# Kernel optimization log

Hardware: AMD Instinct MI355X
Metric: run time of the kernel (lower is better)

The kernel has to match this reference:

```python
import jax, jax.numpy as jnp
import numpy as np

BLOCK = 64
CRIT_TH = 0.5
NEGL_TH = 0.01
TEMP = 1.0
EPS = 1e-6


def setup_inputs() -> dict:
    key = jax.random.key(0)
    kq, kk, kv = jax.random.split(key, 3)
    B, T, H, D = 1, 2048, 8, 64
    q = jax.random.normal(kq, (B, T, H, D), dtype=jnp.float32)
    k = jax.random.normal(kk, (B, T, H, D), dtype=jnp.float32)
    v = jax.random.normal(kv, (B, T, H, D), dtype=jnp.float32)
    return {"q": q, "k": k, "v": v}


def _classify_blocks(qb, kb, D):
    # qb: [B,nq,bs,H,D], kb: [B,nk,bs,H,D]
    q_rep = qb.mean(axis=2)  # [B,nq,H,D]
    k_rep = kb.mean(axis=2)  # [B,nk,H,D]
    bscores = jnp.einsum('bqhd,bkhd->bhqk', q_rep, k_rep) / np.float32(np.sqrt(D))
    ssm = jax.nn.softmax(bscores, axis=-1)
    var = jnp.var(ssm, axis=-1, ddof=1, keepdims=True)  # unbiased, matches torch .var()
    max_scores = bscores.max(axis=-1, keepdims=True)
    imp = var * jnp.maximum(max_scores - bscores.min(), EPS)
    imp_n = (imp - imp.min()) / (imp.max() - imp.min() + EPS)
    crit = imp_n >= CRIT_TH
    negl = imp_n <= NEGL_TH
    marg = (~crit) & (~negl)
    return crit, marg


def reference(q, k, v):
    B, T, H, D = q.shape
    S = k.shape[1]
    nq, nk = T // BLOCK, S // BLOCK  # T,S are multiples of BLOCK (no padding needed)
    dtype = q.dtype

    qb = q.reshape(B, nq, BLOCK, H, D)
    kb = k.reshape(B, nk, BLOCK, H, D)
    vb = v.reshape(B, nk, BLOCK, H, D)

    crit, marg = _classify_blocks(qb, kb, D)  # [B,H,nq,nk] bool
    critf = crit.astype(dtype)
    margf = marg.astype(dtype)

    # ---- exact (critical) blocks: per-block-pair softmax attention ----
    scale = np.float32(1.0 / (np.sqrt(D) * TEMP))
    scores = jnp.einsum('bqthd,bkshd->bhqkts', qb, kb) * scale  # [B,H,nq,nk,bs,bs]
    attn = jax.nn.softmax(scores.astype(jnp.float32), axis=-1).astype(dtype)
    attn_m = attn * critf[:, :, :, :, None, None]
    out_c = jnp.einsum('bhqkts,bkshd->bqthd', attn_m, vb)  # [B,nq,bs,H,D]
    w_c = jnp.einsum('bhqkts->bqth', attn_m)[..., None]    # [B,nq,bs,H,1]

    # ---- linear (marginal) blocks: ELU+1 feature-map attention ----
    qf = jax.nn.elu(qb / TEMP) + 1.0
    kf = jax.nn.elu(kb / TEMP) + 1.0
    kv = jnp.einsum('bkshd,bkshv->bkhdv', kf, vb)              # [B,nk,H,D,D]
    num = jnp.einsum('bqthd,bkhdv->bqkthv', qf, kv)            # [B,nq,nk,bs,H,D]
    k_sum = kf.sum(axis=2)                                     # [B,nk,H,D]
    den = jnp.einsum('bqthd,bkhd->bqkth', qf, k_sum) + EPS     # [B,nq,nk,bs,H]
    out_pair = num / den[..., None]
    out_l = jnp.einsum('bqkthd,bhqk->bqthd', out_pair, margf)
    w_l = jnp.einsum('bqkth,bhqk->bqth', den, margf)[..., None]

    out = (out_c + out_l) / (w_c + w_l + EPS)
    return out.reshape(B, T, H, D)
```

## Files before the change

kernel.cpp:

```cpp
#include <hip/hip_runtime.h>
#include <math.h>

namespace {
constexpr int H  = 8;
constexpr int D  = 64;
constexpr int NB = 32;
constexpr int BS = 64;
constexpr int QST = 68;
}
#define FEPS 1e-6f

typedef unsigned short u16;
typedef unsigned int   u32;
typedef __attribute__((ext_vector_type(8))) short bf16x8;
typedef __attribute__((ext_vector_type(4))) float floatx4;

__device__ __forceinline__ u32 f2bf(float x) {
  union { float f; u32 u; } v; v.f = x;
  return (v.u + 0x7FFFu + ((v.u >> 16) & 1u)) >> 16;
}
__device__ __forceinline__ u32 pk2(float a, float b) { return f2bf(a) | (f2bf(b) << 16); }
#define ELU1(x) ((x) > 0.f ? (x) + 1.f : expf(x))
#define SWZ(row, kblk) ((row)*64 + (((kblk) ^ ((row)&7))*8))

__global__ __launch_bounds__(256) void prep_kernel(const float* __restrict__ q,
                                                   const float* __restrict__ k,
                                                   const float* __restrict__ v,
                                                   float* __restrict__ kvt,
                                                   float* __restrict__ ksum,
                                                   double* __restrict__ qrep,
                                                   double* __restrict__ krep) {
  __shared__ float smem[3*BS*D];
  int bid = blockIdx.x;
  int tid = threadIdx.x;
  if (bid >= 256) {
    double* qred = (double*)smem;
    int r = bid - 256;
    int h = r >> 5, bi = r & 31;
    int d = tid & 63, quarter = tid >> 6;
    double s = 0.0;
    for (int t = quarter*16; t < quarter*16 + 16; ++t)
      s += (double)q[((bi*BS + t)*H + h)*D + d];
    qred[quarter*64 + d] = s;
    __syncthreads();
    if (tid < 64)
      qrep[r*D + tid] = (qred[tid] + qred[64+tid] + qred[128+tid] + qred[192+tid]) * (1.0/64.0);
    return;
  }
  float* kf   = smem;
  float* vv   = smem + BS*D;
  float* kraw = smem + 2*BS*D;
  int h = bid >> 5, ki = bid & 31;
  int sr = tid >> 2, cg = tid & 3;
  const float4* kb = (const float4*)(k + ((ki*BS + sr)*H + h)*D);
  const float4* vb = (const float4*)(v + ((ki*BS + sr)*H + h)*D);
#pragma unroll
  for (int m = 0; m < 4; ++m) {
    float4 kk = kb[cg*4 + m];
    float4 vx = vb[cg*4 + m];
    int c = cg*16 + m*4;
    *(float4*)&kraw[sr*D + c] = kk;
    kf[sr*D + c + 0] = ELU1(kk.x);
    kf[sr*D + c + 1] = ELU1(kk.y);
    kf[sr*D + c + 2] = ELU1(kk.z);
    kf[sr*D + c + 3] = ELU1(kk.w);
    *(float4*)&vv[sr*D + c] = vx;
  }
  __syncthreads();
  int c = tid & 63, dg = tid >> 6, d0 = dg*16;
  float acc[16];
#pragma unroll
  for (int j = 0; j < 16; ++j) acc[j] = 0.f;
#pragma unroll 4
  for (int s2 = 0; s2 < BS; ++s2) {
    float vval = vv[s2*D + c];
    const float4* kr = (const float4*)&kf[s2*D + d0];
    float4 a0 = kr[0], a1 = kr[1], a2 = kr[2], a3 = kr[3];
    acc[0]  += vval*a0.x; acc[1]  += vval*a0.y; acc[2]  += vval*a0.z; acc[3]  += vval*a0.w;
    acc[4]  += vval*a1.x; acc[5]  += vval*a1.y; acc[6]  += vval*a1.z; acc[7]  += vval*a1.w;
    acc[8]  += vval*a2.x; acc[9]  += vval*a2.y; acc[10] += vval*a2.z; acc[11] += vval*a2.w;
    acc[12] += vval*a3.x; acc[13] += vval*a3.y; acc[14] += vval*a3.z; acc[15] += vval*a3.w;
  }
  float* op = kvt + (size_t)bid*4096 + c*64 + d0;
  *(float4*)(op + 0)  = make_float4(acc[0],  acc[1],  acc[2],  acc[3]);
  *(float4*)(op + 4)  = make_float4(acc[4],  acc[5],  acc[6],  acc[7]);
  *(float4*)(op + 8)  = make_float4(acc[8],  acc[9],  acc[10], acc[11]);
  *(float4*)(op + 12) = make_float4(acc[12], acc[13], acc[14], acc[15]);
  if (dg == 0) {
    float ks = 0.f;
    for (int s2 = 0; s2 < BS; ++s2) ks += kf[s2*D + c];
    ksum[bid*D + c] = ks;
    double m = 0.0;
    for (int s2 = 0; s2 < BS; ++s2) m += (double)kraw[s2*D + c];
    krep[bid*D + c] = m * (1.0/64.0);
  }
}

__global__ __launch_bounds__(256) void bscore_kernel(const double* __restrict__ qrep,
                                                     const double* __restrict__ krep,
                                                     double* __restrict__ bsc) {
  int tid = threadIdx.x;
  int lr = tid >> 5, ki = tid & 31;
  int r = blockIdx.x * 8 + lr;
  int h = r >> 5;
  const double* qr = qrep + r*D;
  const double* kr = krep + (h*NB + ki)*D;
  double s = 0.0;
#pragma unroll 16
  for (int d = 0; d < D; ++d) s += qr[d]*kr[d];
  bsc[r*NB + ki] = s * 0.125;
}

__global__ __launch_bounds__(256) void classify3_kernel(const double* __restrict__ bsc,
                                                        int* __restrict__ flags) {
  __shared__ double red[256];
  int tid = threadIdx.x;
  const double* row = bsc + tid*NB;
  double rmax = -1.0e300, rmin = 1.0e300;
#pragma unroll 8
  for (int i = 0; i < NB; ++i) { double b = row[i]; rmax = fmax(rmax, b); rmin = fmin(rmin, b); }
  red[tid] = rmin; __syncthreads();
  for (int s = 128; s > 0; s >>= 1) { if (tid < s) red[tid] = fmin(red[tid], red[tid+s]); __syncthreads(); }
  double gmin = red[0]; __syncthreads();
  double S = 0.0, S2 = 0.0;
#pragma unroll 8
  for (int i = 0; i < NB; ++i) { double e = exp(row[i] - rmax); S += e; S2 += e*e; }
  double invS = 1.0 / S;
  double sp = S * invS;
  double mu = sp * (1.0/32.0);
  double var = (S2*invS*invS - 2.0*mu*sp + 32.0*mu*mu) * (1.0/31.0);
  double rng = rmax - gmin;
  if (rng < 1e-6) rng = 1e-6;
  double imp = var * rng;
  red[tid] = imp; __syncthreads();
  for (int s = 128; s > 0; s >>= 1) { if (tid < s) red[tid] = fmin(red[tid], red[tid+s]); __syncthreads(); }
  double imin = red[0]; __syncthreads();
  red[tid] = imp; __syncthreads();
  for (int s = 128; s > 0; s >>= 1) { if (tid < s) red[tid] = fmax(red[tid], red[tid+s]); __syncthreads(); }
  double imax = red[0];
  double impn = (imp - imin) / (imax - imin + 1e-6);
  flags[tid] = (impn >= 0.5) ? 2 : ((impn <= 0.01) ? 0 : 1);
}

__global__ __launch_bounds__(256) void main_kernel(
    const float* __restrict__ q, const float* __restrict__ k, const float* __restrict__ v,
    const float* __restrict__ kvt, const float* __restrict__ ksum,
    const int* __restrict__ flags, float* __restrict__ out) {
  __shared__ float smem[10304];
  int bid = blockIdx.x;
  int h = bid >> 5, qi = bid & 31;
  int tid = threadIdx.x;
  int row = tid >> 2, cg = tid & 3, c0 = cg*16;
  int lane = tid & 63;
  int flag = flags[bid];

  if (flag == 1) {
    u16*  qfb  = (u16*)smem;
    u16*  kvb  = (u16*)(smem + 2048);
    float* idens = smem + 6144;
    float* wsl   = smem + 8192;
    float* kslc  = smem + 8256;

    {
      const float4* kss = (const float4*)(ksum + (size_t)(h*NB)*D);
      for (int i = tid; i < NB*16; i += 256) ((float4*)kslc)[i] = kss[i];
    }
    float qf[16];
    {
      const float4* qp = (const float4*)(q + ((qi*BS + row)*H + h)*D + c0);
      float4 q0 = qp[0], q1 = qp[1], q2 = qp[2], q3 = qp[3];
      qf[0]=ELU1(q0.x); qf[1]=ELU1(q0.y); qf[2]=ELU1(q0.z); qf[3]=ELU1(q0.w);
      qf[4]=ELU1(q1.x); qf[5]=ELU1(q1.y); qf[6]=ELU1(q1.z); qf[7]=ELU1(q1.w);
      qf[8]=ELU1(q2.x); qf[9]=ELU1(q2.y); qf[10]=ELU1(q2.z); qf[11]=ELU1(q2.w);
      qf[12]=ELU1(q3.x); qf[13]=ELU1(q3.y); qf[14]=ELU1(q3.z); qf[15]=ELU1(q3.w);
      uint4 p0, p1;
      p0.x = pk2(qf[0],qf[1]);  p0.y = pk2(qf[2],qf[3]);
      p0.z = pk2(qf[4],qf[5]);  p0.w = pk2(qf[6],qf[7]);
      p1.x = pk2(qf[8],qf[9]);  p1.y = pk2(qf[10],qf[11]);
      p1.z = pk2(qf[12],qf[13]); p1.w = pk2(qf[14],qf[15]);
      *(uint4*)&qfb[SWZ(row, cg*2)]     = p0;
      *(uint4*)&qfb[SWZ(row, cg*2 + 1)] = p1;
    }
    const float* kvbase = kvt + (size_t)(h*NB)*4096 + row*64 + c0;
    float4 t0, t1, t2, t3;
    {
      const float4* kvp = (const float4*)kvbase;
      t0 = kvp[0]; t1 = kvp[1]; t2 = kvp[2]; t3 = kvp[3];
    }
    __syncthreads();
    {
      float wloc = 0.f;
      for (int ki = 0; ki < NB; ++ki) {
        float pd = 0.f;
#pragma unroll
        for (int j = 0; j < 16; ++j) pd += qf[j] * kslc[ki*64 + c0 + j];
        pd += __shfl_xor(pd, 1, 64);
        pd += __shfl_xor(pd, 2, 64);
        float den = pd + FEPS;
        if (cg == 0) idens[row*32 + ki] = 1.0f / den;
        wloc += den;
      }
      if (cg == 0) wsl[row] = wloc;
    }
    {
      uint4 p0, p1;
      p0.x = pk2(t0.x,t0.y); p0.y = pk2(t0.z,t0.w);
      p0.z = pk2(t1.x,t1.y); p0.w = pk2(t1.z,t1.w);
      p1.x = pk2(t2.x,t2.y); p1.y = pk2(t2.z,t2.w);
      p1.z = pk2(t3.x,t3.y); p1.w = pk2(t3.z,t3.w);
      *(uint4*)&kvb[SWZ(row, cg*2)]     = p0;
      *(uint4*)&kvb[SWZ(row, cg*2 + 1)] = p1;
    }
    int w = tid >> 6, m = lane & 15, quad = lane >> 4;
    bf16x8 aLo = *(const bf16x8*)&qfb[SWZ(w*16 + m, quad)];
    bf16x8 aHi = *(const bf16x8*)&qfb[SWZ(w*16 + m, 4 + quad)];
    int rbase = w*16 + quad*4;
    float acc[16];
#pragma unroll
    for (int j = 0; j < 16; ++j) acc[j] = 0.f;

    for (int ki = 0; ki < NB; ++ki) {
      if (ki + 1 < NB) {
        const float4* kvp = (const float4*)(kvbase + (size_t)(ki+1)*4096);
        t0 = kvp[0]; t1 = kvp[1]; t2 = kvp[2]; t3 = kvp[3];
      }
      __syncthreads();
      const u16* kb = kvb + (ki & 1)*4096;
      float i0 = idens[(rbase + 0)*32 + ki];
      float i1 = idens[(rbase + 1)*32 + ki];
      float i2 = idens[(rbase + 2)*32 + ki];
      float i3 = idens[(rbase + 3)*32 + ki];
      floatx4 zz = {0.f, 0.f, 0.f, 0.f};
#pragma unroll
      for (int t = 0; t < 4; ++t) {
        bf16x8 bLo = *(const bf16x8*)&kb[SWZ(t*16 + m, quad)];
        bf16x8 bHi = *(const bf16x8*)&kb[SWZ(t*16 + m, 4 + quad)];
        floatx4 c4 = __builtin_amdgcn_mfma_f32_16x16x32_bf16(aLo, bLo, zz, 0, 0, 0);
        c4 = __builtin_amdgcn_mfma_f32_16x16x32_bf16(aHi, bHi, c4, 0, 0, 0);
        acc[t*4+0] += c4[0]*i0;
        acc[t*4+1] += c4[1]*i1;
        acc[t*4+2] += c4[2]*i2;
        acc[t*4+3] += c4[3]*i3;
      }
      if (ki + 1 < NB) {
        u16* kw = kvb + ((ki+1) & 1)*4096;
        uint4 p0, p1;
        p0.x = pk2(t0.x,t0.y); p0.y = pk2(t0.z,t0.w);
        p0.z = pk2(t1.x,t1.y); p0.w = pk2(t1.z,t1.w);
        p1.x = pk2(t2.x,t2.y); p1.y = pk2(t2.z,t2.w);
        p1.z = pk2(t3.x,t3.y); p1.w = pk2(t3.z,t3.w);
        *(uint4*)&kw[SWZ(row, cg*2)]     = p0;
        *(uint4*)&kw[SWZ(row, cg*2 + 1)] = p1;
      }
    }
#pragma unroll
    for (int r = 0; r < 4; ++r) {
      float wd = 1.0f / (wsl[rbase + r] + FEPS);
      float* op = out + ((qi*BS + rbase + r)*H + h)*D + m;
#pragma unroll
      for (int t = 0; t < 4; ++t) op[t*16] = acc[t*4+r]*wd;
    }
    return;
  }

  float* bufA = smem;
  float* bufB = smem + 4352;
  float acc[16];
#pragma unroll
  for (int j = 0; j < 16; ++j) acc[j] = 0.f;
  float wsum = 0.f;

  if (flag == 2) {
    const float4* qp = (const float4*)(q + ((qi*BS + row)*H + h)*D);
#pragma unroll
    for (int mm = 0; mm < 4; ++mm) {
      float4 qq = qp[cg*4 + mm];
      int c = c0 + mm*4;
      bufA[row*QST + c + 0] = qq.x*0.125f;
      bufA[row*QST + c + 1] = qq.y*0.125f;
      bufA[row*QST + c + 2] = qq.z*0.125f;
      bufA[row*QST + c + 3] = qq.w*0.125f;
    }
    __syncthreads();
    for (int ki = 0; ki < NB; ++ki) {
      const float4* kp = (const float4*)(k + ((ki*BS + row)*H + h)*D);
#pragma unroll
      for (int mm = 0; mm < 4; ++mm)
        *(float4*)&bufB[row*QST + c0 + mm*4] = kp[cg*4 + mm];
      __syncthreads();
      float sc[16];
#pragma unroll
      for (int j = 0; j < 16; ++j) sc[j] = 0.f;
      for (int d = 0; d < D; ++d) {
        float a = bufA[row*QST + d];
#pragma unroll
        for (int j = 0; j < 16; ++j)
          sc[j] += a * bufB[(c0 + j)*QST + d];
      }
      float mx = sc[0];
#pragma unroll
      for (int j = 1; j < 16; ++j) mx = fmaxf(mx, sc[j]);
      mx = fmaxf(mx, __shfl_xor(mx, 1, 64));
      mx = fmaxf(mx, __shfl_xor(mx, 2, 64));
      float es = 0.f;
      float p[16];
#pragma unroll
      for (int j = 0; j < 16; ++j) { p[j] = expf(sc[j] - mx); es += p[j]; }
      es += __shfl_xor(es, 1, 64);
      es += __shfl_xor(es, 2, 64);
      float inv = 1.0f / es;
#pragma unroll
      for (int j = 0; j < 16; ++j) p[j] *= inv;
      wsum += es * inv;
      __syncthreads();
      const float4* vp = (const float4*)(v + ((ki*BS + row)*H + h)*D);
#pragma unroll
      for (int mm = 0; mm < 4; ++mm)
        *(float4*)&bufB[row*QST + c0 + mm*4] = vp[cg*4 + mm];
      __syncthreads();
      for (int s2 = 0; s2 < BS; ++s2) {
        int g = s2 >> 4, jj = s2 & 15;
        float pv = __shfl(p[jj], (lane & ~3) | g, 64);
        const float4* vr = (const float4*)&bufB[s2*QST + c0];
        float4 a0 = vr[0], a1 = vr[1], a2 = vr[2], a3 = vr[3];
        acc[0]  += pv*a0.x; acc[1]  += pv*a0.y; acc[2]  += pv*a0.z; acc[3]  += pv*a0.w;
        acc[4]  += pv*a1.x; acc[5]  += pv*a1.y; acc[6]  += pv*a1.z; acc[7]  += pv*a1.w;
        acc[8]  += pv*a2.x; acc[9]  += pv*a2.y; acc[10] += pv*a2.z; acc[11] += pv*a2.w;
        acc[12] += pv*a3.x; acc[13] += pv*a3.y; acc[14] += pv*a3.z; acc[15] += pv*a3.w;
      }
      __syncthreads();
    }
  }
  float wd = 1.0f / (wsum + FEPS);
  float* op = out + ((qi*BS + row)*H + h)*D + c0;
  *(float4*)(op + 0)  = make_float4(acc[0]*wd,  acc[1]*wd,  acc[2]*wd,  acc[3]*wd);
  *(float4*)(op + 4)  = make_float4(acc[4]*wd,  acc[5]*wd,  acc[6]*wd,  acc[7]*wd);
  *(float4*)(op + 8)  = make_float4(acc[8]*wd,  acc[9]*wd,  acc[10]*wd, acc[11]*wd);
  *(float4*)(op + 12) = make_float4(acc[12]*wd, acc[13]*wd, acc[14]*wd, acc[15]*wd);
}

extern "C" void kernel_launch(void* const* d_in, const int* in_sizes, int n_in,
                              void* d_out, int out_size, void* d_ws, size_t ws_size,
                              hipStream_t stream) {
  const float* q = (const float*)d_in[0];
  const float* k = (const float*)d_in[1];
  const float* v = (const float*)d_in[2];
  float* out = (float*)d_out;
  char* ws = (char*)d_ws;
  double* qrep = (double*)(ws + 0);
  double* krep = (double*)(ws + 131072);
  int*    flg  = (int*)   (ws + 262144);
  float*  ksw  = (float*) (ws + 263168);
  float*  kvw  = (float*) (ws + 328704);
  double* bsc  = (double*)(ws + 4523008);

  prep_kernel<<<512, 256, 0, stream>>>(q, k, v, kvw, ksw, qrep, krep);
  bscore_kernel<<<32, 256, 0, stream>>>(qrep, krep, bsc);
  classify3_kernel<<<1, 256, 0, stream>>>(bsc, flg);
  main_kernel<<<256, 256, 0, stream>>>(q, k, v, kvw, ksw, flg, out);
}
```

Before: 109.7 us.

## Fuse four kernels into one cooperative kernel with grid syncs

Merges the prep, block-score, classify and main kernels into a single cooperative launch of 256 blocks, separated by two grid-wide barriers. Block scores and row statistics are now computed per block in shared memory. Each block then redoes the global min/max reduction over 256 rows itself, instead of one block classifying everything. The aim is to remove three kernel launch gaps and the intermediate global round-trips; the cost is grid-sync overhead and the constraint that all 256 blocks stay co-resident.

```diff
diff --git a/kernel.cpp b/kernel.cpp
--- a/kernel.cpp
+++ b/kernel.cpp
@@ -1,5 +1,8 @@
 #include <hip/hip_runtime.h>
+#include <hip/hip_cooperative_groups.h>
 #include <math.h>
+
+namespace cg = cooperative_groups;
 
 namespace {
 constexpr int H  = 8;
@@ -23,136 +26,159 @@
 #define ELU1(x) ((x) > 0.f ? (x) + 1.f : expf(x))
 #define SWZ(row, kblk) ((row)*64 + (((kblk) ^ ((row)&7))*8))
 
-__global__ __launch_bounds__(256) void prep_kernel(const float* __restrict__ q,
-                                                   const float* __restrict__ k,
-                                                   const float* __restrict__ v,
-                                                   float* __restrict__ kvt,
-                                                   float* __restrict__ ksum,
-                                                   double* __restrict__ qrep,
-                                                   double* __restrict__ krep) {
-  __shared__ float smem[3*BS*D];
+__global__ __launch_bounds__(256) void fused_kernel(
+    const float* __restrict__ q, const float* __restrict__ k, const float* __restrict__ v,
+    float* __restrict__ kvt, float* __restrict__ ksum, double* __restrict__ krep,
+    double* __restrict__ rowmin, double* __restrict__ rowmax, double* __restrict__ rowvar,
+    float* __restrict__ out) {
+  cg::grid_group grid = cg::this_grid();
+  __shared__ __align__(16) float smem[12288];
   int bid = blockIdx.x;
   int tid = threadIdx.x;
-  if (bid >= 256) {
-    double* qred = (double*)smem;
-    int r = bid - 256;
-    int h = r >> 5, bi = r & 31;
+  int h = bid >> 5, qi = bid & 31;
+
+  {
+    float* kf   = smem;
+    float* vv   = smem + 4096;
+    float* kraw = smem + 8192;
+    int sr = tid >> 2, cgp = tid & 3;
+    const float4* kb = (const float4*)(k + ((qi*BS + sr)*H + h)*D);
+    const float4* vb = (const float4*)(v + ((qi*BS + sr)*H + h)*D);
+#pragma unroll
+    for (int m = 0; m < 4; ++m) {
+      float4 kk = kb[cgp*4 + m];
+      float4 vx = vb[cgp*4 + m];
+      int c = cgp*16 + m*4;
+      *(float4*)&kraw[sr*D + c] = kk;
+      kf[sr*D + c + 0] = ELU1(kk.x);
+      kf[sr*D + c + 1] = ELU1(kk.y);
+      kf[sr*D + c + 2] = ELU1(kk.z);
+      kf[sr*D + c + 3] = ELU1(kk.w);
+      *(float4*)&vv[sr*D + c] = vx;
+    }
+    __syncthreads();
+    int c = tid & 63, dg = tid >> 6, d0 = dg*16;
+    float acc[16];
+#pragma unroll
+    for (int j = 0; j < 16; ++j) acc[j] = 0.f;
+#pragma unroll 4
+    for (int s2 = 0; s2 < BS; ++s2) {
+      float vval = vv[s2*D + c];
+      const float4* kr = (const float4*)&kf[s2*D + d0];
+      float4 a0 = kr[0], a1 = kr[1], a2 = kr[2], a3 = kr[3];
+      acc[0]  += vval*a0.x; acc[1]  += vval*a0.y; acc[2]  += vval*a0.z; acc[3]  += vval*a0.w;
+      acc[4]  += vval*a1.x; acc[5]  += vval*a1.y; acc[6]  += vval*a1.z; acc[7]  += vval*a1.w;
+      acc[8]  += vval*a2.x; acc[9]  += vval*a2.y; acc[10] += vval*a2.z; acc[11] += vval*a2.w;
+      acc[12] += vval*a3.x; acc[13] += vval*a3.y; acc[14] += vval*a3.z; acc[15] += vval*a3.w;
+    }
+    float* op = kvt + (size_t)bid*4096 + c*64 + d0;
+    *(float4*)(op + 0)  = make_float4(acc[0],  acc[1],  acc[2],  acc[3]);
+    *(float4*)(op + 4)  = make_float4(acc[4],  acc[5],  acc[6],  acc[7]);
+    *(float4*)(op + 8)  = make_float4(acc[8],  acc[9],  acc[10], acc[11]);
+    *(float4*)(op + 12) = make_float4(acc[12], acc[13], acc[14], acc[15]);
+    if (dg == 0) {
+      float ks = 0.f;
+      for (int s2 = 0; s2 < BS; ++s2) ks += kf[s2*D + c];
+      ksum[bid*D + c] = ks;
+      double m = 0.0;
+      for (int s2 = 0; s2 < BS; ++s2) m += (double)kraw[s2*D + c];
+      krep[bid*D + c] = m * (1.0/64.0);
+    }
+  }
+  __syncthreads();
+
+  double* qred  = (double*)smem;
+  double* qrepL = (double*)(smem + 512);
+  {
     int d = tid & 63, quarter = tid >> 6;
     double s = 0.0;
     for (int t = quarter*16; t < quarter*16 + 16; ++t)
-      s += (double)q[((bi*BS + t)*H + h)*D + d];
+      s += (double)q[((qi*BS + t)*H + h)*D + d];
     qred[quarter*64 + d] = s;
     __syncthreads();
     if (tid < 64)
-      qrep[r*D + tid] = (qred[tid] + qred[64+tid] + qred[128+tid] + qred[192+tid]) * (1.0/64.0);
-    return;
-  }
-  float* kf   = smem;
-  float* vv   = smem + BS*D;
-  float* kraw = smem + 2*BS*D;
-  int h = bid >> 5, ki = bid & 31;
-  int sr = tid >> 2, cg = tid & 3;
-  const float4* kb = (const float4*)(k + ((ki*BS + sr)*H + h)*D);
-  const float4* vb = (const float4*)(v + ((ki*BS + sr)*H + h)*D);
-#pragma unroll
-  for (int m = 0; m < 4; ++m) {
-    float4 kk = kb[cg*4 + m];
-    float4 vx = vb[cg*4 + m];
-    int c = cg*16 + m*4;
-    *(float4*)&kraw[sr*D + c] = kk;
-    kf[sr*D + c + 0] = ELU1(kk.x);
-    kf[sr*D + c + 1] = ELU1(kk.y);
-    kf[sr*D + c + 2] = ELU1(kk.z);
-    kf[sr*D + c + 3] = ELU1(kk.w);
-    *(float4*)&vv[sr*D + c] = vx;
+      qrepL[tid] = (qred[tid] + qred[64+tid] + qred[128+tid] + qred[192+tid]) * (1.0/64.0);
+    __syncthreads();
+  }
+  __threadfence();
+  grid.sync();
+
+  {
+    double* partb = (double*)(smem + 1024);
+    double* bsrow = (double*)(smem + 1536);
+    int ki = tid & 31, seg = tid >> 5;
+    const double* kr = krep + (size_t)(h*NB + ki)*D + seg*8;
+    double s = 0.0;
+#pragma unroll
+    for (int j = 0; j < 8; ++j) s += qrepL[seg*8 + j] * kr[j];
+    partb[tid] = s;
+    __syncthreads();
+    if (tid < 32) {
+      double s2 = 0.0;
+#pragma unroll
+      for (int g = 0; g < 8; ++g) s2 += partb[g*32 + tid];
+      bsrow[tid] = s2 * 0.125;
+    }
+    __syncthreads();
+    if (tid < 64) {
+      double b = bsrow[tid & 31];
+      double rmax = b, rmin = b;
+#pragma unroll
+      for (int m = 1; m < 32; m <<= 1) {
+        rmax = fmax(rmax, __shfl_xor(rmax, m, 64));
+        rmin = fmin(rmin, __shfl_xor(rmin, m, 64));
+      }
+      double e = exp(b - rmax);
+      double S = e, S2 = e*e;
+#pragma unroll
+      for (int m = 1; m < 32; m <<= 1) {
+        S  += __shfl_xor(S,  m, 64);
+        S2 += __shfl_xor(S2, m, 64);
+      }
+      if (tid == 0) {
+        double invS = 1.0 / S;
+        double sp = S * invS;
+        double mu = sp * (1.0/32.0);
+        double var = (S2*invS*invS - 2.0*mu*sp + 32.0*mu*mu) * (1.0/31.0);
+        rowmin[bid] = rmin;
+        rowmax[bid] = rmax;
+        rowvar[bid] = var;
+      }
+    }
+  }
+  __threadfence();
+  grid.sync();
+
+  int flag;
+  {
+    double* buf  = (double*)smem;
+    double* impL = (double*)(smem + 512);
+    buf[tid] = rowmin[tid];
+    __syncthreads();
+    for (int s = 128; s > 0; s >>= 1) { if (tid < s) buf[tid] = fmin(buf[tid], buf[tid+s]); __syncthreads(); }
+    double gmin = buf[0];
+    __syncthreads();
+    double rng = rowmax[tid] - gmin;
+    if (rng < 1e-6) rng = 1e-6;
+    double imp = rowvar[tid] * rng;
+    impL[tid] = imp;
+    buf[tid] = imp;
+    __syncthreads();
+    for (int s = 128; s > 0; s >>= 1) { if (tid < s) buf[tid] = fmin(buf[tid], buf[tid+s]); __syncthreads(); }
+    double imin = buf[0];
+    __syncthreads();
+    buf[tid] = imp;
+    __syncthreads();
+    for (int s = 128; s > 0; s >>= 1) { if (tid < s) buf[tid] = fmax(buf[tid], buf[tid+s]); __syncthreads(); }
+    double imax = buf[0];
+    __syncthreads();
+    double impn = (impL[bid] - imin) / (imax - imin + 1e-6);
+    flag = (impn >= 0.5) ? 2 : ((impn <= 0.01) ? 0 : 1);
   }
   __syncthreads();
-  int c = tid & 63, dg = tid >> 6, d0 = dg*16;
-  float acc[16];
-#pragma unroll
-  for (int j = 0; j < 16; ++j) acc[j] = 0.f;
-#pragma unroll 4
-  for (int s2 = 0; s2 < BS; ++s2) {
-    float vval = vv[s2*D + c];
-    const float4* kr = (const float4*)&kf[s2*D + d0];
-    float4 a0 = kr[0], a1 = kr[1], a2 = kr[2], a3 = kr[3];
-    acc[0]  += vval*a0.x; acc[1]  += vval*a0.y; acc[2]  += vval*a0.z; acc[3]  += vval*a0.w;
-    acc[4]  += vval*a1.x; acc[5]  += vval*a1.y; acc[6]  += vval*a1.z; acc[7]  += vval*a1.w;
-    acc[8]  += vval*a2.x; acc[9]  += vval*a2.y; acc[10] += vval*a2.z; acc[11] += vval*a2.w;
-    acc[12] += vval*a3.x; acc[13] += vval*a3.y; acc[14] += vval*a3.z; acc[15] += vval*a3.w;
-  }
-  float* op = kvt + (size_t)bid*4096 + c*64 + d0;
-  *(float4*)(op + 0)  = make_float4(acc[0],  acc[1],  acc[2],  acc[3]);
-  *(float4*)(op + 4)  = make_float4(acc[4],  acc[5],  acc[6],  acc[7]);
-  *(float4*)(op + 8)  = make_float4(acc[8],  acc[9],  acc[10], acc[11]);
-  *(float4*)(op + 12) = make_float4(acc[12], acc[13], acc[14], acc[15]);
-  if (dg == 0) {
-    float ks = 0.f;
-    for (int s2 = 0; s2 < BS; ++s2) ks += kf[s2*D + c];
-    ksum[bid*D + c] = ks;
-    double m = 0.0;
-    for (int s2 = 0; s2 < BS; ++s2) m += (double)kraw[s2*D + c];
-    krep[bid*D + c] = m * (1.0/64.0);
-  }
-}
-
-__global__ __launch_bounds__(256) void bscore_kernel(const double* __restrict__ qrep,
-                                                     const double* __restrict__ krep,
-                                                     double* __restrict__ bsc) {
-  int tid = threadIdx.x;
-  int lr = tid >> 5, ki = tid & 31;
-  int r = blockIdx.x * 8 + lr;
-  int h = r >> 5;
-  const double* qr = qrep + r*D;
-  const double* kr = krep + (h*NB + ki)*D;
-  double s = 0.0;
-#pragma unroll 16
-  for (int d = 0; d < D; ++d) s += qr[d]*kr[d];
-  bsc[r*NB + ki] = s * 0.125;
-}
-
-__global__ __launch_bounds__(256) void classify3_kernel(const double* __restrict__ bsc,
-                                                        int* __restrict__ flags) {
-  __shared__ double red[256];
-  int tid = threadIdx.x;
-  const double* row = bsc + tid*NB;
-  double rmax = -1.0e300, rmin = 1.0e300;
-#pragma unroll 8
-  for (int i = 0; i < NB; ++i) { double b = row[i]; rmax = fmax(rmax, b); rmin = fmin(rmin, b); }
-  red[tid] = rmin; __syncthreads();
-  for (int s = 128; s > 0; s >>= 1) { if (tid < s) red[tid] = fmin(red[tid], red[tid+s]); __syncthreads(); }
-  double gmin = red[0]; __syncthreads();
-  double S = 0.0, S2 = 0.0;
-#pragma unroll 8
-  for (int i = 0; i < NB; ++i) { double e = exp(row[i] - rmax); S += e; S2 += e*e; }
-  double invS = 1.0 / S;
-  double sp = S * invS;
-  double mu = sp * (1.0/32.0);
-  double var = (S2*invS*invS - 2.0*mu*sp + 32.0*mu*mu) * (1.0/31.0);
-  double rng = rmax - gmin;
-  if (rng < 1e-6) rng = 1e-6;
-  double imp = var * rng;
-  red[tid] = imp; __syncthreads();
-  for (int s = 128; s > 0; s >>= 1) { if (tid < s) red[tid] = fmin(red[tid], red[tid+s]); __syncthreads(); }
-  double imin = red[0]; __syncthreads();
-  red[tid] = imp; __syncthreads();
-  for (int s = 128; s > 0; s >>= 1) { if (tid < s) red[tid] = fmax(red[tid], red[tid+s]); __syncthreads(); }
-  double imax = red[0];
-  double impn = (imp - imin) / (imax - imin + 1e-6);
-  flags[tid] = (impn >= 0.5) ? 2 : ((impn <= 0.01) ? 0 : 1);
-}
-
-__global__ __launch_bounds__(256) void main_kernel(
-    const float* __restrict__ q, const float* __restrict__ k, const float* __restrict__ v,
-    const float* __restrict__ kvt, const float* __restrict__ ksum,
-    const int* __restrict__ flags, float* __restrict__ out) {
-  __shared__ float smem[10304];
-  int bid = blockIdx.x;
-  int h = bid >> 5, qi = bid & 31;
-  int tid = threadIdx.x;
-  int row = tid >> 2, cg = tid & 3, c0 = cg*16;
+
+  int row = tid >> 2, cgp = tid & 3, c0 = cgp*16;
   int lane = tid & 63;
-  int flag = flags[bid];
 
   if (flag == 1) {
     u16*  qfb  = (u16*)smem;
@@ -178,8 +204,8 @@
       p0.z = pk2(qf[4],qf[5]);  p0.w = pk2(qf[6],qf[7]);
       p1.x = pk2(qf[8],qf[9]);  p1.y = pk2(qf[10],qf[11]);
       p1.z = pk2(qf[12],qf[13]); p1.w = pk2(qf[14],qf[15]);
-      *(uint4*)&qfb[SWZ(row, cg*2)]     = p0;
-      *(uint4*)&qfb[SWZ(row, cg*2 + 1)] = p1;
+      *(uint4*)&qfb[SWZ(row, cgp*2)]     = p0;
+      *(uint4*)&qfb[SWZ(row, cgp*2 + 1)] = p1;
     }
     const float* kvbase = kvt + (size_t)(h*NB)*4096 + row*64 + c0;
     float4 t0, t1, t2, t3;
@@ -197,10 +223,10 @@
         pd += __shfl_xor(pd, 1, 64);
         pd += __shfl_xor(pd, 2, 64);
         float den = pd + FEPS;
-        if (cg == 0) idens[row*32 + ki] = 1.0f / den;
+        if (cgp == 0) idens[row*32 + ki] = 1.0f / den;
         wloc += den;
       }
-      if (cg == 0) wsl[row] = wloc;
+      if (cgp == 0) wsl[row] = wloc;
     }
     {
       uint4 p0, p1;
@@ -208,8 +234,8 @@
       p0.z = pk2(t1.x,t1.y); p0.w = pk2(t1.z,t1.w);
       p1.x = pk2(t2.x,t2.y); p1.y = pk2(t2.z,t2.w);
       p1.z = pk2(t3.x,t3.y); p1.w = pk2(t3.z,t3.w);
-      *(uint4*)&kvb[SWZ(row, cg*2)]     = p0;
-      *(uint4*)&kvb[SWZ(row, cg*2 + 1)] = p1;
+      *(uint4*)&kvb[SWZ(row, cgp*2)]     = p0;
+      *(uint4*)&kvb[SWZ(row, cgp*2 + 1)] = p1;
     }
     int w = tid >> 6, m = lane & 15, quad = lane >> 4;
     bf16x8 aLo = *(const bf16x8*)&qfb[SWZ(w*16 + m, quad)];
@@ -249,8 +275,8 @@
         p0.z = pk2(t1.x,t1.y); p0.w = pk2(t1.z,t1.w);
         p1.x = pk2(t2.x,t2.y); p1.y = pk2(t2.z,t2.w);
         p1.z = pk2(t3.x,t3.y); p1.w = pk2(t3.z,t3.w);
-        *(uint4*)&kw[SWZ(row, cg*2)]     = p0;
-        *(uint4*)&kw[SWZ(row, cg*2 + 1)] = p1;
+        *(uint4*)&kw[SWZ(row, cgp*2)]     = p0;
+        *(uint4*)&kw[SWZ(row, cgp*2 + 1)] = p1;
       }
     }
 #pragma unroll
@@ -274,7 +300,7 @@
     const float4* qp = (const float4*)(q + ((qi*BS + row)*H + h)*D);
 #pragma unroll
     for (int mm = 0; mm < 4; ++mm) {
-      float4 qq = qp[cg*4 + mm];
+      float4 qq = qp[cgp*4 + mm];
       int c = c0 + mm*4;
       bufA[row*QST + c + 0] = qq.x*0.125f;
       bufA[row*QST + c + 1] = qq.y*0.125f;
@@ -286,7 +312,7 @@
       const float4* kp = (const float4*)(k + ((ki*BS + row)*H + h)*D);
 #pragma unroll
       for (int mm = 0; mm < 4; ++mm)
-        *(float4*)&bufB[row*QST + c0 + mm*4] = kp[cg*4 + mm];
+        *(float4*)&bufB[row*QST + c0 + mm*4] = kp[cgp*4 + mm];
       __syncthreads();
       float sc[16];
 #pragma unroll
@@ -316,7 +342,7 @@
       const float4* vp = (const float4*)(v + ((ki*BS + row)*H + h)*D);
 #pragma unroll
       for (int mm = 0; mm < 4; ++mm)
-        *(float4*)&bufB[row*QST + c0 + mm*4] = vp[cg*4 + mm];
+        *(float4*)&bufB[row*QST + c0 + mm*4] = vp[cgp*4 + mm];
       __syncthreads();
       for (int s2 = 0; s2 < BS; ++s2) {
         int g = s2 >> 4, jj = s2 & 15;
@@ -347,15 +373,16 @@
   const float* v = (const float*)d_in[2];
   float* out = (float*)d_out;
   char* ws = (char*)d_ws;
-  double* qrep = (double*)(ws + 0);
-  double* krep = (double*)(ws + 131072);
-  int*    flg  = (int*)   (ws + 262144);
-  float*  ksw  = (float*) (ws + 263168);
-  float*  kvw  = (float*) (ws + 328704);
-  double* bsc  = (double*)(ws + 4523008);
-
-  prep_kernel<<<512, 256, 0, stream>>>(q, k, v, kvw, ksw, qrep, krep);
-  bscore_kernel<<<32, 256, 0, stream>>>(qrep, krep, bsc);
-  classify3_kernel<<<1, 256, 0, stream>>>(bsc, flg);
-  main_kernel<<<256, 256, 0, stream>>>(q, k, v, kvw, ksw, flg, out);
+  float*  kvw  = (float*) (ws + 0);
+  float*  ksw  = (float*) (ws + 4194304);
+  double* krep = (double*)(ws + 4259840);
+  double* rmn  = (double*)(ws + 4390912);
+  double* rmx  = (double*)(ws + 4392960);
+  double* rvr  = (double*)(ws + 4395008);
+
+  void* args[] = {(void*)&q, (void*)&k, (void*)&v,
+                  (void*)&kvw, (void*)&ksw, (void*)&krep,
+                  (void*)&rmn, (void*)&rmx, (void*)&rvr, (void*)&out};
+  hipLaunchCooperativeKernel((const void*)fused_kernel, dim3(256), dim3(256),
+                             args, 0, stream);
 }
```

Result: slower. 191.3 us (+74.4%).
